# Kernel optimization log

Hardware: AMD Instinct MI355X
Metric: run time of the kernel (lower is better)

Reference implementation:

```python
import jax, jax.numpy as jnp
import numpy as np

B, V, K = 128, 128000, 20
_SAMPLING_EPS = 1e-5


def setup_inputs() -> dict:
    key = jax.random.key(0)
    k1, k2, k3 = jax.random.split(key, 3)
    logits = jax.random.normal(k1, (B, V), dtype=jnp.float32)
    temp = jax.random.uniform(k2, (B,), dtype=jnp.float32, minval=0.2, maxval=1.5)
    # every 4th sequence is greedy (temperature < eps)
    temp = jnp.where(jnp.arange(B) % 4 == 0, 0.0, temp)
    # uniform noise in (0,1); exponential noise is q = -log(u)
    u = jax.random.uniform(k3, (B, V), dtype=jnp.float32, minval=1e-7, maxval=1.0)
    return {"logits": logits, "temp": temp, "u": u, "max_num_logprobs": K}


def reference(logits, temp, u, max_num_logprobs):
    # apply_temperature: greedy rows (temp < eps) use temp=1.0
    t = jnp.where(temp < _SAMPLING_EPS, 1.0, temp)
    scaled = logits.astype(jnp.float32) / t[:, None]          # [B, V]
    probs = jax.nn.softmax(scaled, axis=-1)                    # [B, V]
    # greedy sample
    greedy = jnp.argmax(probs, axis=1)                         # [B]
    # random sample via exponential-race (Gumbel-max equivalent): argmax(probs / Exp(1))
    q = -jnp.log(u)                                            # Exp(1) noise
    random_sampled = jnp.argmax(probs / q, axis=1)             # [B]
    sampled = jnp.where(temp < _SAMPLING_EPS, greedy, random_sampled)
    # top-k logprobs
    logprobs = jax.nn.log_softmax(scaled, axis=-1)             # [B, V]
    topk_logprobs, topk_indices = jax.lax.top_k(logprobs, max_num_logprobs)
    return sampled, topk_logprobs, topk_indices
```

## Files before the change

kernel.cpp:

```cpp
#include <hip/hip_runtime.h>
#include <stdint.h>


#define KMAX 20
#define SAMPLING_EPS 1e-5f
#define TAU 3.0f
#define CPB 64
#define LOG2E 1.44269504f
#define LN2 0.69314718f

static __device__ __forceinline__ unsigned int ord32(float v) {
    unsigned int u = __float_as_uint(v);
    return u ^ ((unsigned int)((int)u >> 31) | 0x80000000u);
}
static __device__ __forceinline__ float unord32(unsigned int x) {
    unsigned int u = (x & 0x80000000u) ? (x ^ 0x80000000u) : ~x;
    return __uint_as_float(u);
}
static __device__ __forceinline__ unsigned long long shflxor64(unsigned long long v, int off) {
    int lo = __shfl_xor((int)(unsigned int)v, off, 64);
    int hi = __shfl_xor((int)(unsigned int)(v >> 32), off, 64);
    return ((unsigned long long)(unsigned int)hi << 32) | (unsigned int)lo;
}

__global__ __launch_bounds__(256, 8) void k1_partials(
        const float* __restrict__ logits, const float* __restrict__ u,
        const float* __restrict__ temp,
        unsigned int* __restrict__ wrec,
        unsigned int* __restrict__ cntbuf,
        uint2* __restrict__ candbuf,
        int V, int nsplit) {
    __shared__ int cnt;
    __shared__ uint2 cand[CPB];
    const int b = blockIdx.x;
    const int r = b / nsplit;
    const int sp = b - r * nsplit;
    const int t = threadIdx.x;
    const int lane = t & 63;
    const int w = t >> 6;
    if (t == 0) cnt = 0;
    __syncthreads();

    const float traw = temp[r];
    const bool greedy = traw < SAMPLING_EPS;
    const float inv_t = greedy ? 1.0f : (1.0f / traw);
    const float c = inv_t * LOG2E;

    const int nf4 = V >> 2;
    const int per = (nf4 + nsplit - 1) / nsplit;
    const int f0 = sp * per;
    const int f1 = min(f0 + per, nf4);
    const int f1m = f1 - 1;

    const float4* __restrict__ l4 = (const float4*)(logits + (size_t)r * V);
    const float4* __restrict__ u4 = (const float4*)(u + (size_t)r * V);

    float s = 0.0f;
    float gv = -INFINITY;
    int gcol = 0;

    #define PUSH_CAND(x_, col_)  do { \
        const int idx_ = atomicAdd(&cnt, 1); \
        if (idx_ < CPB) cand[idx_] = make_uint2(__float_as_uint(x_), (unsigned)(col_)); \
    } while (0)

    if (greedy) {
        #define GPROC(x_, col_) do { \
            s += exp2f((x_) * c); \
            if ((x_) >= TAU) PUSH_CAND(x_, col_); \
        } while (0)
        int fb = f0 + t;
        if (fb < f1) {
            float4 lv = l4[fb];
            for (;;) {
                const int fn = fb + 256;
                const float4 nlv = l4[min(fn, f1m)];
                const int colb = fb << 2;
                GPROC(lv.x, colb);
                GPROC(lv.y, colb + 1);
                GPROC(lv.z, colb + 2);
                GPROC(lv.w, colb + 3);
                if (fn >= f1) break;
                fb = fn; lv = nlv;
            }
        }
        #undef GPROC
    } else {
        #define GEXACT(x_, uu_, wm_) \
            ((x_) * c - __log2f(((uu_) > 0.984375f) ? -log1pf(-(wm_)) : -__logf(uu_)))

        {
            const int f = f0 + t;
            const int fc = min(f, f1m);
            const bool act = f < f1;
            const float4 lv = l4[fc];
            const float4 uv = u4[fc];
            const int colb = fc << 2;
            #define PPROC(xr_, uu_, col_) do { \
                const float x_ = act ? (xr_) : -INFINITY; \
                s += exp2f(x_ * c); \
                const float wm_ = 1.0f - (uu_); \
                const float g_ = GEXACT(x_, uu_, wm_); \
                if (g_ > gv) { gv = g_; gcol = (col_); } \
                if (x_ >= TAU) PUSH_CAND(x_, col_); \
            } while (0)
            PPROC(lv.x, uv.x, colb);
            PPROC(lv.y, uv.y, colb + 1);
            PPROC(lv.z, uv.z, colb + 2);
            PPROC(lv.w, uv.w, colb + 3);
            #undef PPROC
        }
        float gmax = gv;
        #pragma unroll
        for (int off = 1; off < 64; off <<= 1) gmax = fmaxf(gmax, __shfl_xor(gmax, off, 64));
        float gvs = gmax - 2e-5f;

        #define MPROC(x_, uu_, col_) do { \
            const float xc_ = (x_) * c; \
            s += exp2f(xc_); \
            const float wm_ = 1.0f - (uu_); \
             \
            const int e_ = (int)(__float_as_uint(wm_) >> 23) - 127; \
            if (xc_ - (float)e_ > gvs) { \
                const float g_ = GEXACT(x_, uu_, wm_); \
                if (g_ > gv) { gv = g_; gcol = (col_); gvs = g_ - 2e-5f; } \
            } \
            if ((x_) >= TAU) PUSH_CAND(x_, col_); \
        } while (0)

        int fb = f0 + t + 256;
        if (fb < f1) {
            float4 lv = l4[fb];
            float4 uv = u4[fb];
            for (;;) {
                const int fn = fb + 256;
                const int fnc = min(fn, f1m);
                const float4 nlv = l4[fnc];
                const float4 nuv = u4[fnc];
                const int colb = fb << 2;
                MPROC(lv.x, uv.x, colb);
                MPROC(lv.y, uv.y, colb + 1);
                MPROC(lv.z, uv.z, colb + 2);
                MPROC(lv.w, uv.w, colb + 3);
                if (fn >= f1) break;
                fb = fn; lv = nlv; uv = nuv;
            }
        }
        #undef MPROC
        #undef GEXACT
    }

    #pragma unroll
    for (int off = 1; off < 64; off <<= 1) s += __shfl_xor(s, off, 64);
    unsigned long long gk = greedy ? 0ull
        : (((unsigned long long)ord32(gv) << 32) | (unsigned int)~(unsigned int)gcol);
    #pragma unroll
    for (int off = 1; off < 64; off <<= 1) {
        const unsigned long long o = shflxor64(gk, off);
        gk = (o > gk) ? o : gk;
    }
    if (lane == 0) {
        unsigned int* rp = wrec + (size_t)(b * 4 + w) * 4;
        rp[0] = __float_as_uint(s);
        rp[1] = __float_as_uint(unord32((unsigned int)(gk >> 32)));
        rp[2] = ~(unsigned int)gk;
        rp[3] = 0u;
    }
    __syncthreads();
    const int cfin = cnt;
    if (t == 0) cntbuf[b] = (unsigned)cfin;
    if (t < min(cfin, CPB)) candbuf[(size_t)b * CPB + t] = cand[t];
}

__global__ __launch_bounds__(64) void k2_finalize(
        const unsigned int* __restrict__ wrec, const unsigned int* __restrict__ cntbuf,
        const uint2* __restrict__ candbuf, const float* __restrict__ logits,
        const float* __restrict__ temp, float* __restrict__ out,
        int B, int V, int K, int nsplit) {
    __shared__ unsigned long long kbuf[512];
    const int r = blockIdx.x;
    const int lane = threadIdx.x;
    const int NW = nsplit * 4;

    const float traw = temp[r];
    const bool greedy = traw < SAMPLING_EPS;
    const float tt = greedy ? 1.0f : traw;

    float s = 0.0f;
    unsigned long long gk = 0ull;
    if (lane < NW) {
        const uint4 rv = ((const uint4*)wrec)[(size_t)r * NW + lane];
        s = __uint_as_float(rv.x);
        gk = ((unsigned long long)ord32(__uint_as_float(rv.y)) << 32) | (unsigned int)~rv.z;
    }
    #pragma unroll
    for (int off = 1; off < 64; off <<= 1) s += __shfl_xor(s, off, 64);
    #pragma unroll
    for (int off = 1; off < 64; off <<= 1) {
        const unsigned long long o = shflxor64(gk, off);
        gk = (o > gk) ? o : gk;
    }
    const float lS = logf(s);

    const int cnt_raw = (lane < nsplit) ? (int)cntbuf[r * nsplit + lane] : 0;
    const int myc = min(cnt_raw, CPB);
    const bool ovf = __ballot(cnt_raw > CPB) != 0ull;
    int incl = myc;
    #pragma unroll
    for (int d = 1; d < 64; d <<= 1) {
        const int o = __shfl_up(incl, d, 64);
        if (lane >= d) incl += o;
    }
    const int T = __shfl(incl, 63, 64);

    const int rec = lane >> 2;
    const int sl0 = lane & 3;
    if (rec < nsplit) {
        const int cbase = __shfl(incl - myc, rec, 64);
        const int ccnt  = __shfl(myc, rec, 64);
        const uint2* cb = candbuf + (size_t)(r * nsplit + rec) * CPB;
        for (int i = sl0; i < ccnt; i += 4) {
            if (cbase + i < 512) {
                const uint2 e = cb[i];
                kbuf[cbase + i] = ((unsigned long long)ord32(__uint_as_float(e.x)) << 32)
                                | (unsigned int)~e.y;
            }
        }
    }
    __syncthreads();

    unsigned long long keys[8];
    #pragma unroll
    for (int jj = 0; jj < 8; ++jj) keys[jj] = 0ull;

    if (!ovf && T >= K && T <= 512) {
        #pragma unroll
        for (int jj = 0; jj < 8; ++jj) {
            const int idx = lane + 64 * jj;
            if (idx < T) keys[jj] = kbuf[idx];
        }
    } else {
        unsigned long long mykey = ((unsigned long long)0x007FFFFFu) << 32;
        unsigned long long minkey = mykey;
        float vmin = -INFINITY;
        const float* lr = logits + (size_t)r * V;
        for (int base = 0; base < V; base += 64) {
            const int i = base + lane;
            const float x = (i < V) ? lr[i] : -INFINITY;
            unsigned long long cm = __ballot((i < V) && (x >= vmin));
            while (cm) {
                const int src = (int)__builtin_ctzll(cm);
                cm &= cm - 1;
                const float cv = __shfl(x, src, 64);
                const int cc = __shfl(i, src, 64);
                const unsigned long long ck =
                    ((unsigned long long)ord32(cv) << 32) | (unsigned int)~(unsigned int)cc;
                if (ck > minkey) {
                    const bool own = (lane < K) && (mykey == minkey);
                    const unsigned long long om = __ballot(own);
                    if (lane == (int)__builtin_ctzll(om)) mykey = ck;
                    unsigned long long mk = (lane < K) ? mykey : ~0ull;
                    #pragma unroll
                    for (int o2 = 1; o2 < 64; o2 <<= 1) {
                        const unsigned long long o = shflxor64(mk, o2);
                        mk = (o < mk) ? o : mk;
                    }
                    minkey = mk;
                    vmin = unord32((unsigned int)(mk >> 32));
                }
            }
        }
        keys[0] = (lane < K) ? mykey : 0ull;
    }

    float* out_s  = out;
    float* out_lp = out + B;
    float* out_ix = out + B + (size_t)B * K;

    unsigned int top1 = 0;
    for (int k = 0; k < K; ++k) {
        unsigned long long loc = keys[0];
        #pragma unroll
        for (int jj = 1; jj < 8; ++jj) loc = (keys[jj] > loc) ? keys[jj] : loc;
        #pragma unroll
        for (int off = 1; off < 64; off <<= 1) {
            const unsigned long long o = shflxor64(loc, off);
            loc = (o > loc) ? o : loc;
        }
        #pragma unroll
        for (int jj = 0; jj < 8; ++jj) if (keys[jj] == loc) keys[jj] = 0ull;
        if (lane == 0) {
            const unsigned int col = ~(unsigned int)loc;
            const float v = unord32((unsigned int)(loc >> 32));
            out_lp[(size_t)r * K + k] = v / tt - lS;
            out_ix[(size_t)r * K + k] = (float)col;
            if (k == 0) top1 = col;
        }
    }
    if (lane == 0) {
        out_s[r] = (float)(greedy ? top1 : (~(unsigned int)gk));
    }
}

extern "C" void kernel_launch(void* const* d_in, const int* in_sizes, int n_in,
                              void* d_out, int out_size, void* d_ws, size_t ws_size,
                              hipStream_t stream) {
    const float* logits = (const float*)d_in[0];
    const float* temp   = (const float*)d_in[1];
    const float* u      = (const float*)d_in[2];
    const int B = in_sizes[1];
    const int V = in_sizes[0] / B;
    int K = (out_size - B) / (2 * B);
    if (K > KMAX) K = KMAX;
    if (K < 1) K = 1;

    int nsplit = 16;
    while (nsplit > 1 && (size_t)B * nsplit * 580 > ws_size) nsplit >>= 1;
    const int blocks = B * nsplit;

    unsigned int* wrec   = (unsigned int*)d_ws;
    unsigned int* cntbuf = wrec + (size_t)blocks * 16;
    uint2*        candbf = (uint2*)(cntbuf + blocks);

    k1_partials<<<dim3(blocks), dim3(256), 0, stream>>>(
        logits, u, temp, wrec, cntbuf, candbf, V, nsplit);
    k2_finalize<<<dim3(B), dim3(64), 0, stream>>>(
        wrec, cntbuf, candbf, logits, temp, (float*)d_out, B, V, K, nsplit);
}
```

Before: 163.0 us.

## Use ratio-domain sampling threshold, unroll two float4s per iteration, fix split count

The random-sampling argmax now tracks probs/q directly as a ratio against a scaled threshold, replacing the log-domain exponent prefilter and the separate first-pass warp max. Each thread processes two float4 chunks per loop iteration with software prefetch, and per-vector max checks gate candidate pushes. The split count becomes a compile-time constant, which removes the runtime division and the workspace-size fallback. The intent is fewer transcendental ops and more memory-level parallelism, at the risk of precision differences in the ratio comparison and workspace overflow if it is too small.

```diff
diff --git a/kernel.cpp b/kernel.cpp
--- a/kernel.cpp
+++ b/kernel.cpp
@@ -7,7 +7,7 @@
 #define TAU 3.0f
 #define CPB 64
 #define LOG2E 1.44269504f
-#define LN2 0.69314718f
+#define NSPLIT 16
 
 static __device__ __forceinline__ unsigned int ord32(float v) {
     unsigned int u = __float_as_uint(v);
@@ -29,12 +29,12 @@
         unsigned int* __restrict__ wrec,
         unsigned int* __restrict__ cntbuf,
         uint2* __restrict__ candbuf,
-        int V, int nsplit) {
+        int V) {
     __shared__ int cnt;
     __shared__ uint2 cand[CPB];
     const int b = blockIdx.x;
-    const int r = b / nsplit;
-    const int sp = b - r * nsplit;
+    const int r = b / NSPLIT;
+    const int sp = b - r * NSPLIT;
     const int t = threadIdx.x;
     const int lane = t & 63;
     const int w = t >> 6;
@@ -43,11 +43,10 @@
 
     const float traw = temp[r];
     const bool greedy = traw < SAMPLING_EPS;
-    const float inv_t = greedy ? 1.0f : (1.0f / traw);
-    const float c = inv_t * LOG2E;
+    const float c = (greedy ? 1.0f : (1.0f / traw)) * LOG2E;
 
     const int nf4 = V >> 2;
-    const int per = (nf4 + nsplit - 1) / nsplit;
+    const int per = (nf4 + NSPLIT - 1) / NSPLIT;
     const int f0 = sp * per;
     const int f1 = min(f0 + per, nf4);
     const int f1m = f1 - 1;
@@ -56,7 +55,7 @@
     const float4* __restrict__ u4 = (const float4*)(u + (size_t)r * V);
 
     float s = 0.0f;
-    float gv = -INFINITY;
+    float G = 0.0f, Gs = 0.0f;
     int gcol = 0;
 
     #define PUSH_CAND(x_, col_)  do { \
@@ -65,95 +64,106 @@
     } while (0)
 
     if (greedy) {
-        #define GPROC(x_, col_) do { \
-            s += exp2f((x_) * c); \
-            if ((x_) >= TAU) PUSH_CAND(x_, col_); \
+        #define GPROC4(lv_, colb_, act_) do { \
+            const float x0 = (act_) ? (lv_).x : -INFINITY; \
+            const float x1 = (act_) ? (lv_).y : -INFINITY; \
+            const float x2 = (act_) ? (lv_).z : -INFINITY; \
+            const float x3 = (act_) ? (lv_).w : -INFINITY; \
+            s += exp2f(x0 * c); s += exp2f(x1 * c); \
+            s += exp2f(x2 * c); s += exp2f(x3 * c); \
+            const float xm = fmaxf(fmaxf(x0, x1), fmaxf(x2, x3)); \
+            if (xm >= TAU) { \
+                if (x0 >= TAU) PUSH_CAND(x0, (colb_)); \
+                if (x1 >= TAU) PUSH_CAND(x1, (colb_) + 1); \
+                if (x2 >= TAU) PUSH_CAND(x2, (colb_) + 2); \
+                if (x3 >= TAU) PUSH_CAND(x3, (colb_) + 3); \
+            } \
         } while (0)
-        int fb = f0 + t;
-        if (fb < f1) {
-            float4 lv = l4[fb];
+        int p = f0 + t;
+        if (p < f1) {
+            float4 la = l4[p];
+            float4 lb = l4[min(p + 256, f1m)];
             for (;;) {
-                const int fn = fb + 256;
-                const float4 nlv = l4[min(fn, f1m)];
-                const int colb = fb << 2;
-                GPROC(lv.x, colb);
-                GPROC(lv.y, colb + 1);
-                GPROC(lv.z, colb + 2);
-                GPROC(lv.w, colb + 3);
-                if (fn >= f1) break;
-                fb = fn; lv = nlv;
+                const int pn = p + 512;
+                const float4 nla = l4[min(pn, f1m)];
+                const float4 nlb = l4[min(pn + 256, f1m)];
+                GPROC4(la, p << 2, true);
+                GPROC4(lb, (p + 256) << 2, (p + 256) < f1);
+                if (pn >= f1) break;
+                p = pn; la = nla; lb = nlb;
             }
         }
-        #undef GPROC
+        #undef GPROC4
     } else {
-        #define GEXACT(x_, uu_, wm_) \
-            ((x_) * c - __log2f(((uu_) > 0.984375f) ? -log1pf(-(wm_)) : -__logf(uu_)))
-
-        {
-            const int f = f0 + t;
-            const int fc = min(f, f1m);
-            const bool act = f < f1;
-            const float4 lv = l4[fc];
-            const float4 uv = u4[fc];
-            const int colb = fc << 2;
-            #define PPROC(xr_, uu_, col_) do { \
-                const float x_ = act ? (xr_) : -INFINITY; \
-                s += exp2f(x_ * c); \
-                const float wm_ = 1.0f - (uu_); \
-                const float g_ = GEXACT(x_, uu_, wm_); \
-                if (g_ > gv) { gv = g_; gcol = (col_); } \
-                if (x_ >= TAU) PUSH_CAND(x_, col_); \
-            } while (0)
-            PPROC(lv.x, uv.x, colb);
-            PPROC(lv.y, uv.y, colb + 1);
-            PPROC(lv.z, uv.z, colb + 2);
-            PPROC(lv.w, uv.w, colb + 3);
-            #undef PPROC
-        }
-        float gmax = gv;
-        #pragma unroll
-        for (int off = 1; off < 64; off <<= 1) gmax = fmaxf(gmax, __shfl_xor(gmax, off, 64));
-        float gvs = gmax - 2e-5f;
-
-        #define MPROC(x_, uu_, col_) do { \
-            const float xc_ = (x_) * c; \
-            s += exp2f(xc_); \
-            const float wm_ = 1.0f - (uu_); \
-             \
-            const int e_ = (int)(__float_as_uint(wm_) >> 23) - 127; \
-            if (xc_ - (float)e_ > gvs) { \
-                const float g_ = GEXACT(x_, uu_, wm_); \
-                if (g_ > gv) { gv = g_; gcol = (col_); gvs = g_ - 2e-5f; } \
+        #define MPROC4(lv_, uv_, colb_, act_) do { \
+            const float x0 = (act_) ? (lv_).x : -INFINITY; \
+            const float x1 = (act_) ? (lv_).y : -INFINITY; \
+            const float x2 = (act_) ? (lv_).z : -INFINITY; \
+            const float x3 = (act_) ? (lv_).w : -INFINITY; \
+            const float e0 = exp2f(x0 * c), e1 = exp2f(x1 * c); \
+            const float e2 = exp2f(x2 * c), e3 = exp2f(x3 * c); \
+            s += e0; s += e1; s += e2; s += e3; \
+            const float wm0 = 1.0f - (uv_).x, wm1 = 1.0f - (uv_).y; \
+            const float wm2 = 1.0f - (uv_).z, wm3 = 1.0f - (uv_).w; \
+            const bool b0 = e0 > Gs * wm0, b1 = e1 > Gs * wm1; \
+            const bool b2 = e2 > Gs * wm2, b3 = e3 > Gs * wm3; \
+            const float xm = fmaxf(fmaxf(x0, x1), fmaxf(x2, x3)); \
+            if (b0 | b1 | b2 | b3 | (xm >= TAU)) { \
+                if (x0 >= TAU) PUSH_CAND(x0, (colb_)); \
+                if (x1 >= TAU) PUSH_CAND(x1, (colb_) + 1); \
+                if (x2 >= TAU) PUSH_CAND(x2, (colb_) + 2); \
+                if (x3 >= TAU) PUSH_CAND(x3, (colb_) + 3); \
+                if (b0) { \
+                    const float uu = (uv_).x; \
+                    const float q = (uu > 0.984375f) ? -log1pf(-wm0) : -__logf(uu); \
+                    const float rr = e0 / q; \
+                    if (rr > G) { G = rr; Gs = G * 0.99902344f; gcol = (colb_); } \
+                } \
+                if (b1) { \
+                    const float uu = (uv_).y; \
+                    const float q = (uu > 0.984375f) ? -log1pf(-wm1) : -__logf(uu); \
+                    const float rr = e1 / q; \
+                    if (rr > G) { G = rr; Gs = G * 0.99902344f; gcol = (colb_) + 1; } \
+                } \
+                if (b2) { \
+                    const float uu = (uv_).z; \
+                    const float q = (uu > 0.984375f) ? -log1pf(-wm2) : -__logf(uu); \
+                    const float rr = e2 / q; \
+                    if (rr > G) { G = rr; Gs = G * 0.99902344f; gcol = (colb_) + 2; } \
+                } \
+                if (b3) { \
+                    const float uu = (uv_).w; \
+                    const float q = (uu > 0.984375f) ? -log1pf(-wm3) : -__logf(uu); \
+                    const float rr = e3 / q; \
+                    if (rr > G) { G = rr; Gs = G * 0.99902344f; gcol = (colb_) + 3; } \
+                } \
             } \
-            if ((x_) >= TAU) PUSH_CAND(x_, col_); \
         } while (0)
-
-        int fb = f0 + t + 256;
-        if (fb < f1) {
-            float4 lv = l4[fb];
-            float4 uv = u4[fb];
+        int p = f0 + t;
+        if (p < f1) {
+            const int pb0 = min(p + 256, f1m);
+            float4 la = l4[p],   ua = u4[p];
+            float4 lb = l4[pb0], ub = u4[pb0];
             for (;;) {
-                const int fn = fb + 256;
-                const int fnc = min(fn, f1m);
-                const float4 nlv = l4[fnc];
-                const float4 nuv = u4[fnc];
-                const int colb = fb << 2;
-                MPROC(lv.x, uv.x, colb);
-                MPROC(lv.y, uv.y, colb + 1);
-                MPROC(lv.z, uv.z, colb + 2);
-                MPROC(lv.w, uv.w, colb + 3);
-                if (fn >= f1) break;
-                fb = fn; lv = nlv; uv = nuv;
+                const int pn = p + 512;
+                const int pnc = min(pn, f1m);
+                const int pnb = min(pn + 256, f1m);
+                const float4 nla = l4[pnc], nlb = l4[pnb];
+                const float4 nua = u4[pnc], nub = u4[pnb];
+                MPROC4(la, ua, p << 2, true);
+                MPROC4(lb, ub, (p + 256) << 2, (p + 256) < f1);
+                if (pn >= f1) break;
+                p = pn; la = nla; lb = nlb; ua = nua; ub = nub;
             }
         }
-        #undef MPROC
-        #undef GEXACT
-    }
+        #undef MPROC4
+    }
+    #undef PUSH_CAND
 
     #pragma unroll
     for (int off = 1; off < 64; off <<= 1) s += __shfl_xor(s, off, 64);
     unsigned long long gk = greedy ? 0ull
-        : (((unsigned long long)ord32(gv) << 32) | (unsigned int)~(unsigned int)gcol);
+        : (((unsigned long long)ord32(G) << 32) | (unsigned int)~(unsigned int)gcol);
     #pragma unroll
     for (int off = 1; off < 64; off <<= 1) {
         const unsigned long long o = shflxor64(gk, off);
@@ -176,11 +186,11 @@
         const unsigned int* __restrict__ wrec, const unsigned int* __restrict__ cntbuf,
         const uint2* __restrict__ candbuf, const float* __restrict__ logits,
         const float* __restrict__ temp, float* __restrict__ out,
-        int B, int V, int K, int nsplit) {
+        int B, int V, int K) {
     __shared__ unsigned long long kbuf[512];
     const int r = blockIdx.x;
     const int lane = threadIdx.x;
-    const int NW = nsplit * 4;
+    const int NW = NSPLIT * 4;
 
     const float traw = temp[r];
     const bool greedy = traw < SAMPLING_EPS;
@@ -202,7 +212,7 @@
     }
     const float lS = logf(s);
 
-    const int cnt_raw = (lane < nsplit) ? (int)cntbuf[r * nsplit + lane] : 0;
+    const int cnt_raw = (lane < NSPLIT) ? (int)cntbuf[r * NSPLIT + lane] : 0;
     const int myc = min(cnt_raw, CPB);
     const bool ovf = __ballot(cnt_raw > CPB) != 0ull;
     int incl = myc;
@@ -215,10 +225,10 @@
 
     const int rec = lane >> 2;
     const int sl0 = lane & 3;
-    if (rec < nsplit) {
+    if (rec < NSPLIT) {
         const int cbase = __shfl(incl - myc, rec, 64);
         const int ccnt  = __shfl(myc, rec, 64);
-        const uint2* cb = candbuf + (size_t)(r * nsplit + rec) * CPB;
+        const uint2* cb = candbuf + (size_t)(r * NSPLIT + rec) * CPB;
         for (int i = sl0; i < ccnt; i += 4) {
             if (cbase + i < 512) {
                 const uint2 e = cb[i];
@@ -314,16 +324,13 @@
     if (K > KMAX) K = KMAX;
     if (K < 1) K = 1;
 
-    int nsplit = 16;
-    while (nsplit > 1 && (size_t)B * nsplit * 580 > ws_size) nsplit >>= 1;
-    const int blocks = B * nsplit;
-
+    const int blocks = B * NSPLIT;
     unsigned int* wrec   = (unsigned int*)d_ws;
     unsigned int* cntbuf = wrec + (size_t)blocks * 16;
     uint2*        candbf = (uint2*)(cntbuf + blocks);
 
     k1_partials<<<dim3(blocks), dim3(256), 0, stream>>>(
-        logits, u, temp, wrec, cntbuf, candbf, V, nsplit);
+        logits, u, temp, wrec, cntbuf, candbf, V);
     k2_finalize<<<dim3(B), dim3(64), 0, stream>>>(
-        wrec, cntbuf, candbf, logits, temp, (float*)d_out, B, V, K, nsplit);
-}
+        wrec, cntbuf, candbf, logits, temp, (float*)d_out, B, V, K);
+}
```

Result: slower. 186.2 us (+14.2%).
